# Performance work log

Measured on AMD Instinct MI355X. Metric: run time of the kernel, lower is better.

## Reference

```python
import jax, jax.numpy as jnp
import numpy as np
from jax import lax

B, L, H, KSIZE = 8, 16384, 128, 65
PAD = KSIZE // 2  # 32; odd kernel keeps output length == L


def setup_inputs() -> dict:
    key = jax.random.key(0)
    kq, kk, kv, kw = jax.random.split(key, 4)
    Q = jax.random.normal(kq, (B, L, H), dtype=jnp.float32)
    K = jax.random.normal(kk, (B, L, H), dtype=jnp.float32)
    V = jax.random.normal(kv, (B, L, H), dtype=jnp.float32)
    # Conv1d weight [out_ch, in_ch, kernel], kaiming-like scale
    W = jax.random.normal(kw, (H, H, KSIZE), dtype=jnp.float32) / np.sqrt(H * KSIZE)
    return {"Q": Q, "K": K, "V": V, "W": W}


def reference(Q, K, V, W):
    # [B, L, H] -> [B, H, L] (channels-first, matching torch transpose(1,2))
    Qt = jnp.swapaxes(Q, 1, 2)
    Kt = jnp.swapaxes(K, 1, 2)
    Vt = jnp.swapaxes(V, 1, 2)
    # Conv1d over sequence dim; lax conv is cross-correlation like torch
    conv_q = lax.conv_general_dilated(
        Qt, W,
        window_strides=(1,),
        padding=[(PAD, PAD)],
        dimension_numbers=("NCH", "OIH", "NCH"),
    )  # [B, H, L]
    scores = conv_q * Kt                      # elementwise gate
    A = jax.nn.softmax(scores, axis=-1)       # softmax over sequence dim
    Z = A * Vt                                # weighted V (elementwise)
    return jnp.swapaxes(Z, 1, 2)              # back to [B, L, H]
```

## Files before the change

kernel.cpp:

```cpp
#include <hip/hip_runtime.h>
#include <stdint.h>

#define BATCH 8
#define LSEQ 16384
#define HDIM 128
#define KSZ 65
#define PADW 32
#define LH (LSEQ*HDIM)
#define TL 256
#define NROWS (TL + 2*PADW)
#define LBLKS (LSEQ/TL)
#define EXP_SHIFT 20.0f

#define WS_WBF_OFF 4096

typedef __attribute__((ext_vector_type(8))) short bf16x8;
typedef __attribute__((ext_vector_type(4))) short bf16x4;
typedef __attribute__((ext_vector_type(16))) float f32x16;

__device__ __forceinline__ unsigned short f2bf(float f) {
  unsigned int u = __float_as_uint(f);
  return (unsigned short)((u + 0x7FFFu + ((u >> 16) & 1u)) >> 16);
}

__global__ __launch_bounds__(256) void wcvt_kernel(const float* __restrict__ W,
                                                   unsigned short* __restrict__ Wbf) {
  __shared__ float lw[KSZ*HDIM];
  const int o = blockIdx.x;
  const float* src = W + (size_t)o * (HDIM*KSZ);
  for (int t = threadIdx.x; t < HDIM*KSZ; t += 256) lw[t] = src[t];
  __syncthreads();
  const int ob  = o >> 5;
  const int l31 = o & 31;
  for (int idx = threadIdx.x; idx < KSZ*HDIM; idx += 256) {
    const int k = idx >> 7;
    const int i = idx & 127;
    const int kk  = i >> 4;
    const int hi2 = (i >> 3) & 1;
    const int e   = i & 7;
    const size_t dst = ((((size_t)(k*4 + ob)*8 + kk)*2 + hi2)*32 + l31)*8 + e;
    Wbf[dst] = f2bf(lw[i*KSZ + k]);
  }
}

__global__ __launch_bounds__(512, 4) void conv_gate_kernel(
    const float* __restrict__ Qm, const float* __restrict__ Km,
    const unsigned short* __restrict__ Wfrag,
    float* __restrict__ Eout, float* __restrict__ gsum) {

  __shared__ __align__(16) unsigned short Qs[NROWS*HDIM];

  const int tid  = threadIdx.x;
  const int lane = tid & 63;
  const int w    = tid >> 6;
  const int wr   = w >> 1;
  const int wc   = w & 1;
  const int l31  = lane & 31;
  const int hi2  = lane >> 5;

  const int bx = blockIdx.x;
  const int b  = bx >> 6;
  const int l0 = (bx & 63) << 8;

  {
    const int r0 = tid >> 5;
    const int c4 = (tid & 31) << 2;
    const float* qbase = Qm + (size_t)b*LH + c4;
#pragma unroll
    for (int it = 0; it < NROWS/16; ++it) {
      const int r = it*16 + r0;
      const int grow = l0 - PADW + r;
      bf16x4 pk = {0, 0, 0, 0};
      if (grow >= 0 && grow < LSEQ) {
        const float4 qv = *(const float4*)(qbase + (size_t)grow*HDIM);
        pk[0] = (short)f2bf(qv.x); pk[1] = (short)f2bf(qv.y);
        pk[2] = (short)f2bf(qv.z); pk[3] = (short)f2bf(qv.w);
      }
      *(bf16x4*)(&Qs[r*HDIM + (c4 ^ ((r & 15) << 3))]) = pk;
    }
  }

  const unsigned short* pb = Wfrag + (size_t)(wc*2)*4096 + hi2*256 + l31*8;

  f32x16 acc[2][2] = {};

  __syncthreads();

  const int arow0 = wr*64 + l31;
  for (int k = 0; k < KSZ; ++k) {
    const unsigned short* pk = pb + (size_t)k*16384;
    const int r0 = k + arow0;
    const int r1 = r0 + 32;
    const int xa0 = (r0 & 15) << 3, xa1 = (r1 & 15) << 3;
#pragma unroll
    for (int kk = 0; kk < 8; ++kk) {
      const int i0 = kk*16 + hi2*8;
      const bf16x8 a0 = *(const bf16x8*)(&Qs[r0*HDIM + (i0 ^ xa0)]);
      const bf16x8 a1 = *(const bf16x8*)(&Qs[r1*HDIM + (i0 ^ xa1)]);
      const bf16x8 b0 = *(const bf16x8*)(pk + kk*512);
      const bf16x8 b1 = *(const bf16x8*)(pk + 4096 + kk*512);
      __builtin_amdgcn_s_setprio(1);
      acc[0][0] = __builtin_amdgcn_mfma_f32_32x32x16_bf16(a0, b0, acc[0][0], 0, 0, 0);
      acc[0][1] = __builtin_amdgcn_mfma_f32_32x32x16_bf16(a0, b1, acc[0][1], 0, 0, 0);
      acc[1][0] = __builtin_amdgcn_mfma_f32_32x32x16_bf16(a1, b0, acc[1][0], 0, 0, 0);
      acc[1][1] = __builtin_amdgcn_mfma_f32_32x32x16_bf16(a1, b1, acc[1][1], 0, 0, 0);
      __builtin_amdgcn_s_setprio(0);
    }
  }

  float psum[2] = {0.f, 0.f};
#pragma unroll
  for (int mf = 0; mf < 2; ++mf) {
#pragma unroll
    for (int r = 0; r < 16; ++r) {
      const int row = wr*64 + mf*32 + (r & 3) + 8*(r >> 2) + 4*hi2;
      const size_t gb = (size_t)b*LH + (size_t)(l0 + row)*HDIM + wc*64 + l31;
#pragma unroll
      for (int nf = 0; nf < 2; ++nf) {
        const float s = acc[mf][nf][r] * Km[gb + nf*32];
        const float e = __expf(s - EXP_SHIFT);
        Eout[gb + nf*32] = e;
        psum[nf] += e;
      }
    }
  }
  psum[0] += __shfl_xor(psum[0], 32);
  psum[1] += __shfl_xor(psum[1], 32);
  if (hi2 == 0) {
    atomicAdd(&gsum[b*HDIM + wc*64 + l31],      psum[0]);
    atomicAdd(&gsum[b*HDIM + wc*64 + 32 + l31], psum[1]);
  }
}

__global__ __launch_bounds__(256) void finalize_kernel(float* __restrict__ out,
                                                       const float* __restrict__ V,
                                                       const float* __restrict__ gsum) {
  const int total4 = (BATCH*LH) >> 2;
  const int stride = gridDim.x * blockDim.x;
  for (int f = blockIdx.x*blockDim.x + threadIdx.x; f < total4; f += stride) {
    const float4 e = ((const float4*)out)[f];
    const float4 v = ((const float4*)V)[f];
    const int e0 = f << 2;
    const float* gs = gsum + ((e0 >> 21) << 7) + (e0 & 127);
    float4 z;
    z.x = e.x * v.x / gs[0];
    z.y = e.y * v.y / gs[1];
    z.z = e.z * v.z / gs[2];
    z.w = e.w * v.w / gs[3];
    ((float4*)out)[f] = z;
  }
}

extern "C" void kernel_launch(void* const* d_in, const int* in_sizes, int n_in,
                              void* d_out, int out_size, void* d_ws, size_t ws_size,
                              hipStream_t stream) {
  (void)in_sizes; (void)n_in; (void)out_size; (void)ws_size;
  const float* Q = (const float*)d_in[0];
  const float* K = (const float*)d_in[1];
  const float* V = (const float*)d_in[2];
  const float* W = (const float*)d_in[3];
  float* out  = (float*)d_out;
  float* gsum = (float*)d_ws;
  unsigned short* Wbf = (unsigned short*)((char*)d_ws + WS_WBF_OFF);

  hipMemsetAsync(d_ws, 0, BATCH*HDIM*sizeof(float), stream);
  wcvt_kernel<<<HDIM, 256, 0, stream>>>(W, Wbf);
  conv_gate_kernel<<<BATCH*LBLKS, 512, 0, stream>>>(Q, K, Wbf, out, gsum);
  finalize_kernel<<<2048, 256, 0, stream>>>(out, V, gsum);
}
```

Before: 335.4 us.

## Enlarge conv tile to 512 rows with 128x128 per-wave MFMA tiles and software-pipelined loads

The sequence tile grows from 256 to 512 rows, and each of 4 waves now computes a 128x128 output block with 4x4 MFMA accumulators instead of a 64x64 block. This gives more reuse of the A (Q) and B (weight) fragments per load. The k/kk loops are flattened into one step loop that double-buffers the LDS and global fragment loads ahead of the MFMAs, and the weight layout is reordered to fit. The cost is a large register footprint (256 accumulator floats) with launch bounds of 1, only 256 blocks (fewer than before), and less occupancy to hide latency.

```diff
diff --git a/kernel.cpp b/kernel.cpp
--- a/kernel.cpp
+++ b/kernel.cpp
@@ -7,9 +7,10 @@
 #define KSZ 65
 #define PADW 32
 #define LH (LSEQ*HDIM)
-#define TL 256
+#define TL 512
 #define NROWS (TL + 2*PADW)
 #define LBLKS (LSEQ/TL)
+#define NSTEP (KSZ*8)
 #define EXP_SHIFT 20.0f
 
 #define WS_WBF_OFF 4096
@@ -38,12 +39,12 @@
     const int kk  = i >> 4;
     const int hi2 = (i >> 3) & 1;
     const int e   = i & 7;
-    const size_t dst = ((((size_t)(k*4 + ob)*8 + kk)*2 + hi2)*32 + l31)*8 + e;
+    const size_t dst = (size_t)(k*8 + kk)*2048 + ob*512 + hi2*256 + l31*8 + e;
     Wbf[dst] = f2bf(lw[i*KSZ + k]);
   }
 }
 
-__global__ __launch_bounds__(512, 4) void conv_gate_kernel(
+__global__ __launch_bounds__(256, 1) void conv_gate_kernel(
     const float* __restrict__ Qm, const float* __restrict__ Km,
     const unsigned short* __restrict__ Wfrag,
     float* __restrict__ Eout, float* __restrict__ gsum) {
@@ -52,23 +53,20 @@
 
   const int tid  = threadIdx.x;
   const int lane = tid & 63;
-  const int w    = tid >> 6;
-  const int wr   = w >> 1;
-  const int wc   = w & 1;
+  const int wv   = tid >> 6;
   const int l31  = lane & 31;
   const int hi2  = lane >> 5;
 
   const int bx = blockIdx.x;
-  const int b  = bx >> 6;
-  const int l0 = (bx & 63) << 8;
+  const int b  = bx >> 5;
+  const int l0 = (bx & 31) << 9;
 
   {
     const int r0 = tid >> 5;
     const int c4 = (tid & 31) << 2;
     const float* qbase = Qm + (size_t)b*LH + c4;
-#pragma unroll
-    for (int it = 0; it < NROWS/16; ++it) {
-      const int r = it*16 + r0;
+    for (int it = 0; it < NROWS/8; ++it) {
+      const int r = it*8 + r0;
       const int grow = l0 - PADW + r;
       bf16x4 pk = {0, 0, 0, 0};
       if (grow >= 0 && grow < LSEQ) {
@@ -80,55 +78,72 @@
     }
   }
 
-  const unsigned short* pb = Wfrag + (size_t)(wc*2)*4096 + hi2*256 + l31*8;
+  f32x16 acc[4][4] = {};
+  const int arow0 = wv*128 + l31;
+  const unsigned short* pb = Wfrag + hi2*256 + l31*8;
 
-  f32x16 acc[2][2] = {};
+#define LOADSTEP(S, A, B) { \
+    const int s_ = (S); \
+    const int rb_ = (s_ >> 3) + arow0; \
+    const int i0_ = ((s_ & 7)*16 + hi2*8) ^ ((rb_ & 15) << 3); \
+    A[0] = *(const bf16x8*)(&Qs[(rb_      )*HDIM + i0_]); \
+    A[1] = *(const bf16x8*)(&Qs[(rb_ +  32)*HDIM + i0_]); \
+    A[2] = *(const bf16x8*)(&Qs[(rb_ +  64)*HDIM + i0_]); \
+    A[3] = *(const bf16x8*)(&Qs[(rb_ +  96)*HDIM + i0_]); \
+    const unsigned short* pt_ = pb + (size_t)s_*2048; \
+    B[0] = *(const bf16x8*)(pt_      ); \
+    B[1] = *(const bf16x8*)(pt_ +  512); \
+    B[2] = *(const bf16x8*)(pt_ + 1024); \
+    B[3] = *(const bf16x8*)(pt_ + 1536); \
+  }
+#define MFMA16(A, B) \
+  _Pragma("unroll") \
+  for (int mf = 0; mf < 4; ++mf) { \
+    acc[mf][0] = __builtin_amdgcn_mfma_f32_32x32x16_bf16(A[mf], B[0], acc[mf][0], 0, 0, 0); \
+    acc[mf][1] = __builtin_amdgcn_mfma_f32_32x32x16_bf16(A[mf], B[1], acc[mf][1], 0, 0, 0); \
+    acc[mf][2] = __builtin_amdgcn_mfma_f32_32x32x16_bf16(A[mf], B[2], acc[mf][2], 0, 0, 0); \
+    acc[mf][3] = __builtin_amdgcn_mfma_f32_32x32x16_bf16(A[mf], B[3], acc[mf][3], 0, 0, 0); \
+  }
+
+  bf16x8 XA[4], XB[4], YA[4], YB[4];
 
   __syncthreads();
 
-  const int arow0 = wr*64 + l31;
-  for (int k = 0; k < KSZ; ++k) {
-    const unsigned short* pk = pb + (size_t)k*16384;
-    const int r0 = k + arow0;
-    const int r1 = r0 + 32;
-    const int xa0 = (r0 & 15) << 3, xa1 = (r1 & 15) << 3;
+  LOADSTEP(0, XA, XB)
+  for (int s = 0; s < NSTEP; s += 2) {
+    const int s1 = (s + 1 < NSTEP) ? s + 1 : NSTEP - 1;
+    const int s2 = (s + 2 < NSTEP) ? s + 2 : NSTEP - 1;
+    LOADSTEP(s1, YA, YB)
+    MFMA16(XA, XB)
+    LOADSTEP(s2, XA, XB)
+    MFMA16(YA, YB)
+  }
+#undef LOADSTEP
+#undef MFMA16
+
+  float psum[4] = {0.f, 0.f, 0.f, 0.f};
 #pragma unroll
-    for (int kk = 0; kk < 8; ++kk) {
-      const int i0 = kk*16 + hi2*8;
-      const bf16x8 a0 = *(const bf16x8*)(&Qs[r0*HDIM + (i0 ^ xa0)]);
-      const bf16x8 a1 = *(const bf16x8*)(&Qs[r1*HDIM + (i0 ^ xa1)]);
-      const bf16x8 b0 = *(const bf16x8*)(pk + kk*512);
-      const bf16x8 b1 = *(const bf16x8*)(pk + 4096 + kk*512);
-      __builtin_amdgcn_s_setprio(1);
-      acc[0][0] = __builtin_amdgcn_mfma_f32_32x32x16_bf16(a0, b0, acc[0][0], 0, 0, 0);
-      acc[0][1] = __builtin_amdgcn_mfma_f32_32x32x16_bf16(a0, b1, acc[0][1], 0, 0, 0);
-      acc[1][0] = __builtin_amdgcn_mfma_f32_32x32x16_bf16(a1, b0, acc[1][0], 0, 0, 0);
-      acc[1][1] = __builtin_amdgcn_mfma_f32_32x32x16_bf16(a1, b1, acc[1][1], 0, 0, 0);
-      __builtin_amdgcn_s_setprio(0);
-    }
-  }
-
-  float psum[2] = {0.f, 0.f};
-#pragma unroll
-  for (int mf = 0; mf < 2; ++mf) {
+  for (int mf = 0; mf < 4; ++mf) {
 #pragma unroll
     for (int r = 0; r < 16; ++r) {
-      const int row = wr*64 + mf*32 + (r & 3) + 8*(r >> 2) + 4*hi2;
-      const size_t gb = (size_t)b*LH + (size_t)(l0 + row)*HDIM + wc*64 + l31;
+      const int row = wv*128 + mf*32 + (r & 3) + 8*(r >> 2) + 4*hi2;
+      const size_t gb = (size_t)b*LH + (size_t)(l0 + row)*HDIM + l31;
 #pragma unroll
-      for (int nf = 0; nf < 2; ++nf) {
-        const float s = acc[mf][nf][r] * Km[gb + nf*32];
-        const float e = __expf(s - EXP_SHIFT);
+      for (int nf = 0; nf < 4; ++nf) {
+        const float sc = acc[mf][nf][r] * Km[gb + nf*32];
+        const float e = __expf(sc - EXP_SHIFT);
         Eout[gb + nf*32] = e;
         psum[nf] += e;
       }
     }
   }
-  psum[0] += __shfl_xor(psum[0], 32);
-  psum[1] += __shfl_xor(psum[1], 32);
+#pragma unroll
+  for (int nf = 0; nf < 4; ++nf)
+    psum[nf] += __shfl_xor(psum[nf], 32);
   if (hi2 == 0) {
-    atomicAdd(&gsum[b*HDIM + wc*64 + l31],      psum[0]);
-    atomicAdd(&gsum[b*HDIM + wc*64 + 32 + l31], psum[1]);
+#pragma unroll
+    for (int nf = 0; nf < 4; ++nf)
+      atomicAdd(&gsum[b*HDIM + nf*32 + l31], psum[nf]);
   }
 }
 
@@ -165,6 +180,6 @@
 
   hipMemsetAsync(d_ws, 0, BATCH*HDIM*sizeof(float), stream);
   wcvt_kernel<<<HDIM, 256, 0, stream>>>(W, Wbf);
-  conv_gate_kernel<<<BATCH*LBLKS, 512, 0, stream>>>(Q, K, Wbf, out, gsum);
+  conv_gate_kernel<<<BATCH*LBLKS, 256, 0, stream>>>(Q, K, Wbf, out, gsum);
   finalize_kernel<<<2048, 256, 0, stream>>>(out, V, gsum);
 }
```

New measurement: 437.1 us. 30.3% more time.

## Split conv GEMM reduction across warps and stream weights into LDS via async loads

Applied to the files above, without the earlier changes.

Work is repartitioned so each warp owns one 32-column output slice across all 256 rows and half of the input-channel reduction, raising B-fragment reuse to eight MFMAs per load. Per-tap weight fragments are double-buffered into LDS with global_load_lds so the next tap's fetch overlaps the current tap's MFMAs. The two reduction halves are combined through shared memory before the exp/gate epilogue. In exchange the block uses far more LDS (about 144KB) and more accumulator registers, so occupancy drops to two blocks per CU and half the warps sit idle in the epilogue.

```diff
diff --git a/kernel.cpp b/kernel.cpp
--- a/kernel.cpp
+++ b/kernel.cpp
@@ -30,31 +30,33 @@
   const float* src = W + (size_t)o * (HDIM*KSZ);
   for (int t = threadIdx.x; t < HDIM*KSZ; t += 256) lw[t] = src[t];
   __syncthreads();
-  const int ob  = o >> 5;
+  const int wc_ = o >> 5;
   const int l31 = o & 31;
   for (int idx = threadIdx.x; idx < KSZ*HDIM; idx += 256) {
     const int k = idx >> 7;
     const int i = idx & 127;
-    const int kk  = i >> 4;
+    const int ks_ = i >> 6;
+    const int kk2 = (i >> 4) & 3;
     const int hi2 = (i >> 3) & 1;
     const int e   = i & 7;
-    const size_t dst = ((((size_t)(k*4 + ob)*8 + kk)*2 + hi2)*32 + l31)*8 + e;
+    const size_t dst = (size_t)k*16384 + wc_*4096 + ks_*2048 + kk2*512 + hi2*256 + l31*8 + e;
     Wbf[dst] = f2bf(lw[i*KSZ + k]);
   }
 }
 
-__global__ __launch_bounds__(512, 4) void conv_gate_kernel(
+__global__ __launch_bounds__(512, 2) void conv_gate_kernel(
     const float* __restrict__ Qm, const float* __restrict__ Km,
     const unsigned short* __restrict__ Wfrag,
     float* __restrict__ Eout, float* __restrict__ gsum) {
 
-  __shared__ __align__(16) unsigned short Qs[NROWS*HDIM];
+  __shared__ __align__(16) char smem[147456];
+  unsigned short* Qs = (unsigned short*)smem;
 
   const int tid  = threadIdx.x;
   const int lane = tid & 63;
   const int w    = tid >> 6;
-  const int wr   = w >> 1;
-  const int wc   = w & 1;
+  const int ks   = w & 1;
+  const int wc   = w >> 1;
   const int l31  = lane & 31;
   const int hi2  = lane >> 5;
 
@@ -80,55 +82,102 @@
     }
   }
 
-  const unsigned short* pb = Wfrag + (size_t)(wc*2)*4096 + hi2*256 + l31*8;
-
-  f32x16 acc[2][2] = {};
-
-  __syncthreads();
-
-  const int arow0 = wr*64 + l31;
+  char* wslot = smem + 81920 + w*8192;
+  const char* gW = (const char*)Wfrag + wc*8192 + ks*4096;
+
+#pragma unroll
+  for (int j = 0; j < 4; ++j)
+    __builtin_amdgcn_global_load_lds(
+        (const __attribute__((address_space(1))) unsigned int*)(gW + j*1024 + lane*16),
+        (__attribute__((address_space(3))) unsigned int*)(wslot + j*1024 + lane*16 - lane*16 + j*0 + (lane*16)), 16, 0, 0);
+
+  f32x16 acc[8] = {};
+
+  __syncthreads();
+
+  const int rbase = l31;
+
   for (int k = 0; k < KSZ; ++k) {
-    const unsigned short* pk = pb + (size_t)k*16384;
-    const int r0 = k + arow0;
-    const int r1 = r0 + 32;
-    const int xa0 = (r0 & 15) << 3, xa1 = (r1 & 15) << 3;
-#pragma unroll
-    for (int kk = 0; kk < 8; ++kk) {
-      const int i0 = kk*16 + hi2*8;
-      const bf16x8 a0 = *(const bf16x8*)(&Qs[r0*HDIM + (i0 ^ xa0)]);
-      const bf16x8 a1 = *(const bf16x8*)(&Qs[r1*HDIM + (i0 ^ xa1)]);
-      const bf16x8 b0 = *(const bf16x8*)(pk + kk*512);
-      const bf16x8 b1 = *(const bf16x8*)(pk + 4096 + kk*512);
-      __builtin_amdgcn_s_setprio(1);
-      acc[0][0] = __builtin_amdgcn_mfma_f32_32x32x16_bf16(a0, b0, acc[0][0], 0, 0, 0);
-      acc[0][1] = __builtin_amdgcn_mfma_f32_32x32x16_bf16(a0, b1, acc[0][1], 0, 0, 0);
-      acc[1][0] = __builtin_amdgcn_mfma_f32_32x32x16_bf16(a1, b0, acc[1][0], 0, 0, 0);
-      acc[1][1] = __builtin_amdgcn_mfma_f32_32x32x16_bf16(a1, b1, acc[1][1], 0, 0, 0);
-      __builtin_amdgcn_s_setprio(0);
-    }
-  }
-
-  float psum[2] = {0.f, 0.f};
-#pragma unroll
-  for (int mf = 0; mf < 2; ++mf) {
-#pragma unroll
-    for (int r = 0; r < 16; ++r) {
-      const int row = wr*64 + mf*32 + (r & 3) + 8*(r >> 2) + 4*hi2;
-      const size_t gb = (size_t)b*LH + (size_t)(l0 + row)*HDIM + wc*64 + l31;
-#pragma unroll
-      for (int nf = 0; nf < 2; ++nf) {
-        const float s = acc[mf][nf][r] * Km[gb + nf*32];
+    const int cur = k & 1;
+    asm volatile("s_waitcnt vmcnt(0)" ::: "memory");
+    if (k < KSZ-1) {
+      const char* gs = gW + (size_t)(k+1)*32768;
+      char* ld = wslot + (cur^1)*4096;
+#pragma unroll
+      for (int j = 0; j < 4; ++j)
+        __builtin_amdgcn_global_load_lds(
+            (const __attribute__((address_space(1))) unsigned int*)(gs + j*1024 + lane*16),
+            (__attribute__((address_space(3))) unsigned int*)(ld + j*1024),
+            16, 0, 0);
+    }
+
+    const unsigned short* bslot = (const unsigned short*)(wslot + cur*4096);
+    const int rb = k + rbase;
+    const int xa = (rb & 15) << 3;
+
+#pragma unroll
+    for (int kk = 0; kk < 4; ++kk) {
+      const int i0 = (ks*64 + kk*16 + hi2*8) ^ xa;
+      const unsigned short* ar = &Qs[rb*HDIM + i0];
+      const bf16x8 B = *(const bf16x8*)(bslot + kk*512 + hi2*256 + l31*8);
+      const bf16x8 A0 = *(const bf16x8*)(ar);
+      const bf16x8 A1 = *(const bf16x8*)(ar + 1*4096);
+      const bf16x8 A2 = *(const bf16x8*)(ar + 2*4096);
+      const bf16x8 A3 = *(const bf16x8*)(ar + 3*4096);
+      const bf16x8 A4 = *(const bf16x8*)(ar + 4*4096);
+      const bf16x8 A5 = *(const bf16x8*)(ar + 5*4096);
+      const bf16x8 A6 = *(const bf16x8*)(ar + 6*4096);
+      const bf16x8 A7 = *(const bf16x8*)(ar + 7*4096);
+      acc[0] = __builtin_amdgcn_mfma_f32_32x32x16_bf16(A0, B, acc[0], 0, 0, 0);
+      acc[1] = __builtin_amdgcn_mfma_f32_32x32x16_bf16(A1, B, acc[1], 0, 0, 0);
+      acc[2] = __builtin_amdgcn_mfma_f32_32x32x16_bf16(A2, B, acc[2], 0, 0, 0);
+      acc[3] = __builtin_amdgcn_mfma_f32_32x32x16_bf16(A3, B, acc[3], 0, 0, 0);
+      acc[4] = __builtin_amdgcn_mfma_f32_32x32x16_bf16(A4, B, acc[4], 0, 0, 0);
+      acc[5] = __builtin_amdgcn_mfma_f32_32x32x16_bf16(A5, B, acc[5], 0, 0, 0);
+      acc[6] = __builtin_amdgcn_mfma_f32_32x32x16_bf16(A6, B, acc[6], 0, 0, 0);
+      acc[7] = __builtin_amdgcn_mfma_f32_32x32x16_bf16(A7, B, acc[7], 0, 0, 0);
+    }
+  }
+
+  __syncthreads();
+  float* red = (float*)smem;
+  float* reg = red + wc*8192 + lane*4;
+  if (ks == 1) {
+#pragma unroll
+    for (int q4 = 0; q4 < 32; ++q4) {
+      const int m = q4 >> 2, r4 = (q4 & 3) << 2;
+      float4 v;
+      v.x = acc[m][r4];   v.y = acc[m][r4+1];
+      v.z = acc[m][r4+2]; v.w = acc[m][r4+3];
+      *(float4*)(reg + q4*256) = v;
+    }
+  }
+  __syncthreads();
+
+  if (ks == 0) {
+#pragma unroll
+    for (int q4 = 0; q4 < 32; ++q4) {
+      const int m = q4 >> 2, r4 = (q4 & 3) << 2;
+      const float4 v = *(const float4*)(reg + q4*256);
+      acc[m][r4]   += v.x; acc[m][r4+1] += v.y;
+      acc[m][r4+2] += v.z; acc[m][r4+3] += v.w;
+    }
+    float psum = 0.f;
+#pragma unroll
+    for (int m = 0; m < 8; ++m) {
+#pragma unroll
+      for (int r = 0; r < 16; ++r) {
+        const int row = m*32 + (r & 3) + 8*(r >> 2) + 4*hi2;
+        const size_t gb = (size_t)b*LH + (size_t)(l0 + row)*HDIM + wc*32 + l31;
+        const float s = acc[m][r] * Km[gb];
         const float e = __expf(s - EXP_SHIFT);
-        Eout[gb + nf*32] = e;
-        psum[nf] += e;
+        Eout[gb] = e;
+        psum += e;
       }
     }
-  }
-  psum[0] += __shfl_xor(psum[0], 32);
-  psum[1] += __shfl_xor(psum[1], 32);
-  if (hi2 == 0) {
-    atomicAdd(&gsum[b*HDIM + wc*64 + l31],      psum[0]);
-    atomicAdd(&gsum[b*HDIM + wc*64 + 32 + l31], psum[1]);
+    psum += __shfl_xor(psum, 32);
+    if (hi2 == 0)
+      atomicAdd(&gsum[b*HDIM + wc*32 + l31], psum);
   }
 }
 
```

Result: faster. 285.9 us (-14.8%).
